# Kernel optimization log

Measured on AMD Instinct MI355X. Metric: run time of the kernel, lower is better.

The kernel has to match this reference:

```python
import jax, jax.numpy as jnp
import numpy as np
from jax import lax

EPS = 1e-08


def setup_inputs() -> dict:
    key = jax.random.key(0)
    k1, k2, k3 = jax.random.split(key, 3)
    B, I, O, H, W_, K = 16, 512, 512, 32, 32, 3
    x = jax.random.normal(k1, (B, I, H, W_), dtype=jnp.float32)
    s = jax.random.uniform(k2, (B, I), dtype=jnp.float32)
    weight = jax.random.normal(k3, (O, I, K, K), dtype=jnp.float32)
    return {"x": x, "s": s, "weight": weight}


def reference(x, s, weight):
    # x: [B, I, H, W], s: [B, I], weight: [O, I, kH, kW]
    B, I, H, Wd = x.shape
    O = weight.shape[0]
    # Per-sample modulated weights: [B, O, I, kH, kW]
    # (faithful to source: the weight_scale multiply is dead code, overwritten)
    Wm = s[:, None, :, None, None] * weight[None]
    # Demodulation: L2-normalize each per-sample output filter
    sigma = jnp.sqrt(jnp.sum(Wm * Wm, axis=(2, 3, 4), keepdims=True) + EPS)
    Wm = Wm / sigma
    # Grouped conv with groups = batch_size (same trick as torch source)
    x_g = x.reshape(1, B * I, H, Wd)
    W_g = Wm.reshape(B * O, I, *weight.shape[-2:])
    out = lax.conv_general_dilated(
        x_g, W_g,
        window_strides=(1, 1),
        padding='SAME',
        feature_group_count=B,
        dimension_numbers=('NCHW', 'OIHW', 'NCHW'),
    )
    return out.reshape(B, O, out.shape[-2], out.shape[-1])
```

## Files before the change

### kernel.cpp

```cpp
#include <hip/hip_runtime.h>
#include <hip/hip_bf16.h>
#include <stdint.h>

#define BATCH 16
#define CIN   512
#define COUT  512
#define HH    32
#define WW    32
#define HP    34
#define HWN   1024
#define EPS_  1e-8f

#define NTILES 72
#define SLOT   16384
#define LDS_BYTES (5*SLOT)

typedef __attribute__((ext_vector_type(8))) short bf16x8;
typedef __attribute__((ext_vector_type(4))) float f32x4;
typedef __attribute__((address_space(1))) void gvoid;
typedef __attribute__((address_space(3))) void lvoid;

#define XS_OFF    0
#define XS_BYTES  (BATCH*HP*HP*CIN*2)
#define WT_OFF    (XS_OFF + XS_BYTES)
#define WT_BYTES  (9*COUT*CIN*2)
#define ISG_OFF   (WT_OFF + WT_BYTES)

__global__ __launch_bounds__(256)
void prep_all(const float* __restrict__ x, const float* __restrict__ s,
              const float* __restrict__ w,
              __hip_bfloat16* __restrict__ xs, __hip_bfloat16* __restrict__ wt,
              float* __restrict__ isg) {
  __shared__ __align__(16) char smem[35328];
  const int bid = blockIdx.x;
  const int tid = threadIdx.x;

  if (bid < BATCH * 34) {
    unsigned short (*tile)[520] = (unsigned short (*)[520])smem;
    float* ssh = (float*)(smem + 33280);
    const int hp = bid % 34;
    const int b  = bid / 34;
    __hip_bfloat16* rowbase = xs + (((size_t)(b * HP + hp)) * HP) * CIN;

    if (hp == 0 || hp == 33) {
      for (int j = tid; j < HP * CIN / 8; j += 256)
        ((int4*)rowbase)[j] = make_int4(0, 0, 0, 0);
      return;
    }
    if (tid < 64)        ((int4*)rowbase)[tid] = make_int4(0, 0, 0, 0);
    else if (tid < 128)  ((int4*)(rowbase + 33 * CIN))[tid - 64] = make_int4(0, 0, 0, 0);

    ssh[tid]       = s[b * CIN + tid];
    ssh[256 + tid] = s[b * CIN + 256 + tid];
    __syncthreads();

    const int h = hp - 1;
    const int r = tid >> 3;
    const int c = tid & 7;
    const float* xbase = x + (size_t)b * CIN * HWN + h * WW;
#pragma unroll
    for (int p = 0; p < 16; ++p) {
      int i = p * 32 + r;
      float4 v = *(const float4*)(xbase + (size_t)i * HWN + c * 4);
      float sc = ssh[i];
#pragma unroll
      for (int j = 0; j < 4; ++j) {
        float f = ((const float*)&v)[j] * sc;
        __hip_bfloat16 hb = __float2bfloat16(f);
        tile[c * 4 + j][i] = *(unsigned short*)&hb;
      }
    }
    __syncthreads();

    const int wq = tid >> 3;
    const int i0 = (tid & 7) * 64;
    __hip_bfloat16* dst = rowbase + (wq + 1) * CIN + i0;
    const int4* src = (const int4*)&tile[wq][i0];
#pragma unroll
    for (int q = 0; q < 8; ++q)
      ((int4*)dst)[q] = src[q];
  } else {
    float* s2  = (float*)smem;
    float (*red)[4] = (float (*)[4])(smem + 32768);
    const int o = bid - BATCH * 34;
    for (int j = tid; j < BATCH * CIN; j += 256) {
      float v = s[j];
      s2[j] = v * v;
    }
    float ss[2];
#pragma unroll
    for (int u = 0; u < 2; ++u) {
      int i = tid + u * 256;
      const float* wp = w + ((size_t)o * CIN + i) * 9;
      float acc = 0.f;
#pragma unroll
      for (int k = 0; k < 9; ++k) {
        float v = wp[k];
        acc += v * v;
        wt[(size_t)k * COUT * CIN + o * CIN + i] = __float2bfloat16(v);
      }
      ss[u] = acc;
    }
    __syncthreads();
    float accb[16];
#pragma unroll
    for (int b = 0; b < 16; ++b) accb[b] = 0.f;
#pragma unroll
    for (int u = 0; u < 2; ++u) {
      int i = tid + u * 256;
      float q = ss[u];
#pragma unroll
      for (int b = 0; b < 16; ++b) accb[b] += q * s2[b * CIN + i];
    }
#pragma unroll
    for (int b = 0; b < 16; ++b) {
#pragma unroll
      for (int off = 32; off; off >>= 1) accb[b] += __shfl_xor(accb[b], off);
      if ((tid & 63) == 0) red[b][tid >> 6] = accb[b];
    }
    __syncthreads();
    if (tid < 16) {
      float tot = red[tid][0] + red[tid][1] + red[tid][2] + red[tid][3];
      isg[tid * COUT + o] = 1.0f / sqrtf(tot + EPS_);
    }
  }
}

__global__ __launch_bounds__(256, 2)
void conv_cnt(const __hip_bfloat16* __restrict__ xs,
              const __hip_bfloat16* __restrict__ wt,
              const float* __restrict__ isg,
              float* __restrict__ out) {
  extern __shared__ __align__(16) char lds[];
  char* ldsA = lds;
  char* ldsB = lds + 2 * SLOT;

  const int bid = blockIdx.x;
  const int nt = bid & 7;
  const int mt = (bid >> 3) & 3;
  const int b  = bid >> 5;
  const int m0  = mt * 128;
  const int hw0 = nt * 128;

  const int t  = threadIdx.x;
  const int wv = t >> 6;
  const int l  = t & 63;
  const int wr = wv >> 1;
  const int wc = wv & 1;
  const int segbase = wv * 4;

  int baseA[4], baseB[4];
#pragma unroll
  for (int q = 0; q < 4; ++q) {
    int seg = segbase + q;
    int r = seg * 8 + (l >> 3);
    int swz = (l & 7) ^ (l >> 3);
    baseA[q] = (m0 + r) * CIN + swz * 8;
    int n_abs = hw0 + r;
    int hB = n_abs >> 5, wB = n_abs & 31;
    baseB[q] = ((b * HP + hB) * HP + wB) * CIN + swz * 8;
  }

  int offA[2][4], offB[2][4];
#pragma unroll
  for (int kk = 0; kk < 2; ++kk) {
#pragma unroll
    for (int f = 0; f < 4; ++f) {
      int slot = ((kk * 4) + (l >> 4)) ^ (l & 7);
      offA[kk][f] = (wr * 64 + f * 16 + (l & 15)) * 128 + slot * 16;
      offB[kk][f] = (wc * 64 + f * 16 + (l & 15)) * 128 + slot * 16;
    }
  }

  f32x4 acc[4][4];
#pragma unroll
  for (int m = 0; m < 4; ++m)
#pragma unroll
    for (int n = 0; n < 4; ++n)
      acc[m][n] = (f32x4){0.f, 0.f, 0.f, 0.f};

#define STAGE_A(tt, sl)                                                     \
  {                                                                         \
    int tc_ = (tt) < NTILES ? (tt) : NTILES - 1;                            \
    int tap_ = tc_ >> 3, ic_ = tc_ & 7;                                     \
    int gA_ = tap_ * (COUT * CIN) + ic_ * 64;                               \
    char* dA_ = ldsA + (sl) * SLOT;                                         \
    _Pragma("unroll")                                                       \
    for (int q = 0; q < 4; ++q)                                             \
      __builtin_amdgcn_global_load_lds(                                     \
          (gvoid*)(const void*)(wt + gA_ + baseA[q]),                       \
          (lvoid*)(dA_ + (segbase + q) * 1024), 16, 0, 0);                  \
  }

#define STAGE_B(tt, sl)                                                     \
  {                                                                         \
    int tc_ = (tt) < NTILES ? (tt) : NTILES - 1;                            \
    int tap_ = tc_ >> 3, ic_ = tc_ & 7;                                     \
    int kh_ = (tap_ * 11) >> 5;                                             \
    int kw_ = tap_ - kh_ * 3;                                               \
    int gB_ = (kh_ * HP + kw_) * CIN + ic_ * 64;                            \
    char* dB_ = ldsB + (sl) * SLOT;                                         \
    _Pragma("unroll")                                                       \
    for (int q = 0; q < 4; ++q)                                             \
      __builtin_amdgcn_global_load_lds(                                     \
          (gvoid*)(const void*)(xs + gB_ + baseB[q]),                       \
          (lvoid*)(dB_ + (segbase + q) * 1024), 16, 0, 0);                  \
  }

#define KK_PHASE(kk, pA, pB)                                                \
  {                                                                         \
    bf16x8 af[4], bfr[4];                                                   \
    _Pragma("unroll")                                                       \
    for (int f = 0; f < 4; ++f) af[f]  = *(const bf16x8*)((pA) + offA[kk][f]); \
    _Pragma("unroll")                                                       \
    for (int f = 0; f < 4; ++f) bfr[f] = *(const bf16x8*)((pB) + offB[kk][f]); \
    __builtin_amdgcn_s_setprio(1);                                          \
    _Pragma("unroll")                                                       \
    for (int m = 0; m < 4; ++m)                                             \
      _Pragma("unroll")                                                     \
      for (int n = 0; n < 4; ++n)                                           \
        acc[m][n] = __builtin_amdgcn_mfma_f32_16x16x32_bf16(                \
            af[m], bfr[n], acc[m][n], 0, 0, 0);                             \
    __builtin_amdgcn_s_setprio(0);                                          \
  }

  STAGE_B(0, 0);
  STAGE_A(0, 0);
  STAGE_B(1, 1);
  asm volatile("s_waitcnt vmcnt(4)" ::: "memory");
  __builtin_amdgcn_sched_barrier(0);
  __builtin_amdgcn_s_barrier();
  __builtin_amdgcn_sched_barrier(0);

  int bB = 0;
  int sB2 = 2;
#pragma unroll 1
  for (int tt = 0; tt < NTILES; ++tt) {
    STAGE_A(tt + 1, (tt + 1) & 1);
    const char* pA = ldsA + (tt & 1) * SLOT;
    const char* pB = ldsB + bB * SLOT;
    KK_PHASE(0, pA, pB);
    STAGE_B(tt + 2, sB2);
    KK_PHASE(1, pA, pB);
    asm volatile("s_waitcnt lgkmcnt(0)" ::: "memory");
    asm volatile("s_waitcnt vmcnt(4)" ::: "memory");
    __builtin_amdgcn_sched_barrier(0);
    __builtin_amdgcn_s_barrier();
    __builtin_amdgcn_sched_barrier(0);
    bB  = (bB  == 2) ? 0 : bB + 1;
    sB2 = (sB2 == 2) ? 0 : sB2 + 1;
  }
  asm volatile("s_waitcnt vmcnt(0)" ::: "memory");

#pragma unroll
  for (int m = 0; m < 4; ++m) {
#pragma unroll
    for (int j = 0; j < 4; ++j) {
      int o = m0 + wr * 64 + m * 16 + (l >> 4) * 4 + j;
      float sg = isg[b * COUT + o];
      float* orow = out + ((size_t)(b * COUT + o)) * HWN + hw0 + wc * 64 + (l & 15);
#pragma unroll
      for (int n = 0; n < 4; ++n)
        orow[n * 16] = acc[m][n][j] * sg;
    }
  }
}

extern "C" void kernel_launch(void* const* d_in, const int* in_sizes, int n_in,
                              void* d_out, int out_size, void* d_ws, size_t ws_size,
                              hipStream_t stream) {
  const float* x = (const float*)d_in[0];
  const float* s = (const float*)d_in[1];
  const float* w = (const float*)d_in[2];
  float* out = (float*)d_out;
  char* ws = (char*)d_ws;
  __hip_bfloat16* xs  = (__hip_bfloat16*)(ws + XS_OFF);
  __hip_bfloat16* wt  = (__hip_bfloat16*)(ws + WT_OFF);
  float*          isg = (float*)(ws + ISG_OFF);

  (void)hipFuncSetAttribute((const void*)conv_cnt,
                            hipFuncAttributeMaxDynamicSharedMemorySize, LDS_BYTES);

  hipLaunchKernelGGL(prep_all, dim3(BATCH * 34 + COUT), dim3(256), 0, stream,
                     x, s, w, xs, wt, isg);
  hipLaunchKernelGGL(conv_cnt, dim3(512), dim3(256), LDS_BYTES, stream,
                     xs, wt, isg, out);
}
```

Measured before the change: 164.3 us.

## Enlarge conv tile to 256x128 per block and remap block order

Doubles the M tile of the implicit-GEMM conv from 128 to 256 output channels per block. Each wave now computes 128x64 with 8x4 MFMA accumulators, and the grid is halved to 256 blocks at one block per CU. Block indices are also permuted so neighbouring blocks spread across batch and tile positions, likely for L2/XCD locality. The aim is more data reuse per LDS load and fewer redundant activation loads, at the cost of higher register pressure and one wave group per SIMD, which leaves less latency hiding.

After: 198.3 us. +20.7%, slower.

```diff
diff --git a/kernel.cpp b/kernel.cpp
--- a/kernel.cpp
+++ b/kernel.cpp
@@ -12,8 +12,9 @@
 #define EPS_  1e-8f
 
 #define NTILES 72
-#define SLOT   16384
-#define LDS_BYTES (5*SLOT)
+#define SLOTA_ 32768
+#define SLOTB_ 16384
+#define LDS_BYTES (2*SLOTA_ + 3*SLOTB_)
 
 typedef __attribute__((ext_vector_type(8))) short bf16x8;
 typedef __attribute__((ext_vector_type(4))) float f32x4;
@@ -126,20 +127,21 @@
   }
 }
 
-__global__ __launch_bounds__(256, 2)
-void conv_cnt(const __hip_bfloat16* __restrict__ xs,
-              const __hip_bfloat16* __restrict__ wt,
-              const float* __restrict__ isg,
-              float* __restrict__ out) {
+__global__ __launch_bounds__(256, 1)
+void conv_w(const __hip_bfloat16* __restrict__ xs,
+            const __hip_bfloat16* __restrict__ wt,
+            const float* __restrict__ isg,
+            float* __restrict__ out) {
   extern __shared__ __align__(16) char lds[];
   char* ldsA = lds;
-  char* ldsB = lds + 2 * SLOT;
+  char* ldsB = lds + 2 * SLOTA_;
 
   const int bid = blockIdx.x;
-  const int nt = bid & 7;
-  const int mt = (bid >> 3) & 3;
-  const int b  = bid >> 5;
-  const int m0  = mt * 128;
+  const int lin = (bid & 7) * 32 + (bid >> 3);
+  const int b  = lin >> 4;
+  const int mt = (lin >> 3) & 1;
+  const int nt = lin & 7;
+  const int m0  = mt * 256;
   const int hw0 = nt * 128;
 
   const int t  = threadIdx.x;
@@ -147,34 +149,41 @@
   const int l  = t & 63;
   const int wr = wv >> 1;
   const int wc = wv & 1;
-  const int segbase = wv * 4;
-
-  int baseA[4], baseB[4];
+
+  int baseA[8], baseB[4];
+  const int swz = (l & 7) ^ (l >> 3);
+#pragma unroll
+  for (int q = 0; q < 8; ++q) {
+    int r = (wv * 8 + q) * 8 + (l >> 3);
+    baseA[q] = (m0 + r) * CIN + swz * 8;
+  }
 #pragma unroll
   for (int q = 0; q < 4; ++q) {
-    int seg = segbase + q;
-    int r = seg * 8 + (l >> 3);
-    int swz = (l & 7) ^ (l >> 3);
-    baseA[q] = (m0 + r) * CIN + swz * 8;
+    int r = (wv * 4 + q) * 8 + (l >> 3);
     int n_abs = hw0 + r;
     int hB = n_abs >> 5, wB = n_abs & 31;
     baseB[q] = ((b * HP + hB) * HP + wB) * CIN + swz * 8;
   }
 
-  int offA[2][4], offB[2][4];
+  int offA[2][8], offB[2][4];
 #pragma unroll
   for (int kk = 0; kk < 2; ++kk) {
-#pragma unroll
-    for (int f = 0; f < 4; ++f) {
-      int slot = ((kk * 4) + (l >> 4)) ^ (l & 7);
-      offA[kk][f] = (wr * 64 + f * 16 + (l & 15)) * 128 + slot * 16;
-      offB[kk][f] = (wc * 64 + f * 16 + (l & 15)) * 128 + slot * 16;
-    }
-  }
-
-  f32x4 acc[4][4];
-#pragma unroll
-  for (int m = 0; m < 4; ++m)
+    int slot16;
+#pragma unroll
+    for (int mf = 0; mf < 8; ++mf) {
+      slot16 = ((kk * 4) + (l >> 4)) ^ (l & 7);
+      offA[kk][mf] = (wr * 128 + mf * 16 + (l & 15)) * 128 + slot16 * 16;
+    }
+#pragma unroll
+    for (int nf = 0; nf < 4; ++nf) {
+      slot16 = ((kk * 4) + (l >> 4)) ^ (l & 7);
+      offB[kk][nf] = (wc * 64 + nf * 16 + (l & 15)) * 128 + slot16 * 16;
+    }
+  }
+
+  f32x4 acc[8][4];
+#pragma unroll
+  for (int m = 0; m < 8; ++m)
 #pragma unroll
     for (int n = 0; n < 4; ++n)
       acc[m][n] = (f32x4){0.f, 0.f, 0.f, 0.f};
@@ -184,12 +193,12 @@
     int tc_ = (tt) < NTILES ? (tt) : NTILES - 1;                            \
     int tap_ = tc_ >> 3, ic_ = tc_ & 7;                                     \
     int gA_ = tap_ * (COUT * CIN) + ic_ * 64;                               \
-    char* dA_ = ldsA + (sl) * SLOT;                                         \
-    _Pragma("unroll")                                                       \
-    for (int q = 0; q < 4; ++q)                                             \
+    char* dA_ = ldsA + (sl) * SLOTA_;                                       \
+    _Pragma("unroll")                                                       \
+    for (int q = 0; q < 8; ++q)                                             \
       __builtin_amdgcn_global_load_lds(                                     \
           (gvoid*)(const void*)(wt + gA_ + baseA[q]),                       \
-          (lvoid*)(dA_ + (segbase + q) * 1024), 16, 0, 0);                  \
+          (lvoid*)(dA_ + (wv * 8 + q) * 1024), 16, 0, 0);                   \
   }
 
 #define STAGE_B(tt, sl)                                                     \
@@ -199,24 +208,24 @@
     int kh_ = (tap_ * 11) >> 5;                                             \
     int kw_ = tap_ - kh_ * 3;                                               \
     int gB_ = (kh_ * HP + kw_) * CIN + ic_ * 64;                            \
-    char* dB_ = ldsB + (sl) * SLOT;                                         \
+    char* dB_ = ldsB + (sl) * SLOTB_;                                       \
     _Pragma("unroll")                                                       \
     for (int q = 0; q < 4; ++q)                                             \
       __builtin_amdgcn_global_load_lds(                                     \
           (gvoid*)(const void*)(xs + gB_ + baseB[q]),                       \
-          (lvoid*)(dB_ + (segbase + q) * 1024), 16, 0, 0);                  \
+          (lvoid*)(dB_ + (wv * 4 + q) * 1024), 16, 0, 0);                   \
   }
 
 #define KK_PHASE(kk, pA, pB)                                                \
   {                                                                         \
-    bf16x8 af[4], bfr[4];                                                   \
-    _Pragma("unroll")                                                       \
-    for (int f = 0; f < 4; ++f) af[f]  = *(const bf16x8*)((pA) + offA[kk][f]); \
+    bf16x8 af[8], bfr[4];                                                   \
+    _Pragma("unroll")                                                       \
+    for (int f = 0; f < 8; ++f) af[f]  = *(const bf16x8*)((pA) + offA[kk][f]); \
     _Pragma("unroll")                                                       \
     for (int f = 0; f < 4; ++f) bfr[f] = *(const bf16x8*)((pB) + offB[kk][f]); \
     __builtin_amdgcn_s_setprio(1);                                          \
     _Pragma("unroll")                                                       \
-    for (int m = 0; m < 4; ++m)                                             \
+    for (int m = 0; m < 8; ++m)                                             \
       _Pragma("unroll")                                                     \
       for (int n = 0; n < 4; ++n)                                           \
         acc[m][n] = __builtin_amdgcn_mfma_f32_16x16x32_bf16(                \
@@ -237,8 +246,8 @@
 #pragma unroll 1
   for (int tt = 0; tt < NTILES; ++tt) {
     STAGE_A(tt + 1, (tt + 1) & 1);
-    const char* pA = ldsA + (tt & 1) * SLOT;
-    const char* pB = ldsB + bB * SLOT;
+    const char* pA = ldsA + (tt & 1) * SLOTA_;
+    const char* pB = ldsB + bB * SLOTB_;
     KK_PHASE(0, pA, pB);
     STAGE_B(tt + 2, sB2);
     KK_PHASE(1, pA, pB);
@@ -253,10 +262,10 @@
   asm volatile("s_waitcnt vmcnt(0)" ::: "memory");
 
 #pragma unroll
-  for (int m = 0; m < 4; ++m) {
+  for (int m = 0; m < 8; ++m) {
 #pragma unroll
     for (int j = 0; j < 4; ++j) {
-      int o = m0 + wr * 64 + m * 16 + (l >> 4) * 4 + j;
+      int o = m0 + wr * 128 + m * 16 + (l >> 4) * 4 + j;
       float sg = isg[b * COUT + o];
       float* orow = out + ((size_t)(b * COUT + o)) * HWN + hw0 + wc * 64 + (l & 15);
 #pragma unroll
@@ -278,11 +287,11 @@
   __hip_bfloat16* wt  = (__hip_bfloat16*)(ws + WT_OFF);
   float*          isg = (float*)(ws + ISG_OFF);
 
-  (void)hipFuncSetAttribute((const void*)conv_cnt,
+  (void)hipFuncSetAttribute((const void*)conv_w,
                             hipFuncAttributeMaxDynamicSharedMemorySize, LDS_BYTES);
 
   hipLaunchKernelGGL(prep_all, dim3(BATCH * 34 + COUT), dim3(256), 0, stream,
                      x, s, w, xs, wt, isg);
-  hipLaunchKernelGGL(conv_cnt, dim3(512), dim3(256), LDS_BYTES, stream,
+  hipLaunchKernelGGL(conv_w, dim3(256), dim3(256), LDS_BYTES, stream,
                      xs, wt, isg, out);
 }
```
